# Kernel tuning notes

Measured on AMD Instinct MI355X. Metric: run time of the kernel, lower is better.

Reference implementation:

```python
import jax, jax.numpy as jnp
import numpy as np

N_ENT = 20000
N_REL = 24
N_EDGE = 200000
BATCH = 64
N_RULES = 32
RULE_LEN = 2


def setup_inputs() -> dict:
    key = jax.random.key(0)
    ks = jax.random.split(key, 9)
    return {
        "all_h": jax.random.randint(ks[0], (BATCH,), 0, N_ENT, dtype=jnp.int32),
        "all_r": jnp.zeros((BATCH,), dtype=jnp.int32),  # query relation = 0 for all queries
        "edges_to_remove": jax.random.randint(ks[1], (BATCH,), 0, N_EDGE, dtype=jnp.int32),
        "edge_heads": jax.random.randint(ks[2], (N_EDGE,), 0, N_ENT, dtype=jnp.int32),
        "edge_rels": jax.random.randint(ks[3], (N_EDGE,), 0, N_REL, dtype=jnp.int32),
        "edge_tails": jax.random.randint(ks[4], (N_EDGE,), 0, N_ENT, dtype=jnp.int32),
        "rule_bodies": jax.random.randint(ks[5], (N_RULES, RULE_LEN), 0, N_REL, dtype=jnp.int32),
        "rule_weights": jax.random.normal(ks[6], (N_RULES,), dtype=jnp.float32),
        "bias": jax.random.normal(ks[7], (N_ENT,), dtype=jnp.float32),
    }


def reference(all_h, all_r, edges_to_remove, edge_heads, edge_rels, edge_tails,
              rule_bodies, rule_weights, bias):
    n_ent = bias.shape[0]
    rule_len = rule_bodies.shape[1]
    b = all_h.shape[0]

    # edge keep-mask (edges_to_remove are dropped from the graph for this query batch)
    keep = jnp.ones((edge_heads.shape[0],), jnp.float32).at[edges_to_remove].set(0.0)

    # grounding start state: one-hot of query heads, [B, N]
    x0 = jax.nn.one_hot(all_h, n_ent, dtype=jnp.float32)

    def propagate(x, r):
        # one hop of rule grounding: route counts along edges with relation r
        w = keep * (edge_rels == r).astype(jnp.float32)      # [E]
        contrib = x[:, edge_heads] * w[None, :]              # [B, E] gather
        # scatter-add into tail entities -> [B, N]
        return jax.ops.segment_sum(contrib.T, edge_tails, num_segments=n_ent).T

    def per_rule(carry, rule):
        score, mask = carry
        body, weight = rule
        x = x0
        for l in range(rule_len):
            x = propagate(x, body[l])
        return (score + x * weight, mask + x), None

    zeros = jnp.zeros((b, n_ent), jnp.float32)
    (score, mask), _ = jax.lax.scan(per_rule, (zeros, zeros), (rule_bodies, rule_weights))

    # entity_feature == 'bias' path: score + bias, mask all True.
    # (If mask.sum()==0, score is also all-zero, so score+bias == mask+bias and
    #  (1-mask).bool() == ones: the two torch branches coincide for 'bias'.)
    out_score = score + bias[None, :]
    out_mask = jnp.ones_like(mask, dtype=bool)
    return out_score, out_mask
```

## Files before the change

### kernel.cpp

```cpp
#include <hip/hip_runtime.h>


namespace {
constexpr int kNEnt    = 20000;
constexpr int kNRel    = 24;
constexpr int kNEdge   = 200000;
constexpr int kBatch   = 64;
constexpr int kNRules  = 32;
constexpr int kWSz     = kNRel * kNRel;
constexpr int kScore4  = kBatch * kNEnt / 4;
constexpr int kOut4    = 2 * kScore4;
constexpr int kB1      = 1024;
constexpr int kT       = 256;
}

__global__ void __launch_bounds__(kT) k_init_frontier(
        const int* __restrict__ all_h,
        const int* __restrict__ rem,
        const int* __restrict__ eh,
        const int* __restrict__ er,
        const int* __restrict__ et,
        const float* __restrict__ bias,
        float* __restrict__ out,
        int* __restrict__ headptr,
        unsigned* __restrict__ nodeNext,
        unsigned long long* __restrict__ nodeBm) {
    __shared__ int sh[kBatch];
    __shared__ int srem[kBatch];
    const int t = threadIdx.x;
    if (t < kBatch) sh[t] = all_h[t];
    else if (t < 2 * kBatch) srem[t - kBatch] = rem[t - kBatch];
    __syncthreads();
    const int gid = blockIdx.x * kT + t;
    constexpr int stride = kB1 * kT;

    for (int i = gid; i < kOut4; i += stride) {
        if (i < kScore4)
            ((float4*)out)[i] = ((const float4*)bias)[i % (kNEnt / 4)];
        else
            ((float4*)out)[i] = make_float4(1.f, 1.f, 1.f, 1.f);
    }

    for (int e = gid; e < kNEdge; e += stride) {
        int h = eh[e];
        unsigned long long bm = 0ull;
        for (int b = 0; b < kBatch; b++)
            bm |= (unsigned long long)(sh[b] == h) << b;
        if (!bm) continue;
        bool removed = false;
        for (int i = 0; i < kBatch; i++) removed |= (srem[i] == e);
        if (removed) continue;
        int tail = et[e];
        int r1   = er[e];
        int old  = atomicExch(&headptr[tail], e + 1);
        unsigned nxt = (old <= 0) ? 0u : (unsigned)old;
        nodeNext[e] = nxt | ((unsigned)r1 << 24);
        nodeBm[e]   = bm;
    }
}

__global__ void __launch_bounds__(kT) k_hop2(
        const int* __restrict__ rem,
        const int* __restrict__ eh,
        const int* __restrict__ er,
        const int* __restrict__ et,
        const int* __restrict__ rb,
        const float* __restrict__ rw,
        const int* __restrict__ headptr,
        const unsigned* __restrict__ nodeNext,
        const unsigned long long* __restrict__ nodeBm,
        float* __restrict__ out) {
    __shared__ float sW[kWSz];
    __shared__ int srem[kBatch];
    const int t = threadIdx.x;
    for (int i = t; i < kWSz; i += kT) sW[i] = 0.f;
    if (t < kBatch) srem[t] = rem[t];
    __syncthreads();
    if (t < kNRules)
        atomicAdd(&sW[rb[2 * t] * kNRel + rb[2 * t + 1]], rw[t]);
    __syncthreads();

    int e = blockIdx.x * kT + t;
    if (e >= kNEdge) return;
    int h = eh[e];
    int p = headptr[h];
    if (p <= 0) return;
    bool removed = false;
    for (int i = 0; i < kBatch; i++) removed |= (srem[i] == e);
    if (removed) return;
    int r2 = er[e];
    int t2 = et[e];
    while (p > 0) {
        int e1 = p - 1;
        unsigned nx           = nodeNext[e1];
        unsigned long long bm = nodeBm[e1];
        float w = sW[((nx >> 24) & 31u) * kNRel + r2];
        while (bm) {
            int b = __ffsll(bm) - 1;
            bm &= bm - 1;
            atomicAdd(&out[b * kNEnt + t2], w);
        }
        p = (int)(nx & 0xFFFFFFu);
    }
}

extern "C" void kernel_launch(void* const* d_in, const int* in_sizes, int n_in,
                              void* d_out, int out_size, void* d_ws, size_t ws_size,
                              hipStream_t stream) {
    const int*   all_h = (const int*)d_in[0];
    const int*   rem   = (const int*)d_in[2];
    const int*   eh    = (const int*)d_in[3];
    const int*   er    = (const int*)d_in[4];
    const int*   et    = (const int*)d_in[5];
    const int*   rb    = (const int*)d_in[6];
    const float* rw    = (const float*)d_in[7];
    const float* bias  = (const float*)d_in[8];
    float* out = (float*)d_out;

    char* ws = (char*)d_ws;
    int*                headptr  = (int*)(ws + 0);
    unsigned*           nodeNext = (unsigned*)(ws + 81920);
    unsigned long long* nodeBm   = (unsigned long long*)(ws + 881920);

    hipLaunchKernelGGL(k_init_frontier, dim3(kB1), dim3(kT), 0, stream,
                       all_h, rem, eh, er, et, bias, out,
                       headptr, nodeNext, nodeBm);
    hipLaunchKernelGGL(k_hop2, dim3((kNEdge + kT - 1) / kT), dim3(kT), 0, stream,
                       rem, eh, er, et, rb, rw, headptr, nodeNext, nodeBm, out);
}
```

Baseline: 83.46 us.

## Fuse frontier build and hop-2 into one persistent kernel with grid barrier

Merges the two kernels into a single launch of 512 blocks that uses a software grid-wide barrier (atomic counter plus magic-flag reset) between building the first-hop linked lists and the second-hop scatter. This removes one kernel launch and the gap between the two kernels. In exchange it depends on all 512 blocks being co-resident. The barrier reset races, because block 0 zeroes the counter while other blocks may already be incrementing it, and on later calls the magic flag is already set, so blocks can pass before the reset. A spin limit bounds hangs but can let blocks proceed early and read incomplete lists.

```diff
diff --git a/kernel.cpp b/kernel.cpp
--- a/kernel.cpp
+++ b/kernel.cpp
@@ -8,40 +8,57 @@
 constexpr int kBatch   = 64;
 constexpr int kNRules  = 32;
 constexpr int kWSz     = kNRel * kNRel;
+constexpr int kBlocks  = 512;
+constexpr int kT       = 256;
+constexpr int kGT      = kBlocks * kT;
 constexpr int kScore4  = kBatch * kNEnt / 4;
 constexpr int kOut4    = 2 * kScore4;
-constexpr int kB1      = 1024;
-constexpr int kT       = 256;
+constexpr unsigned kMagic     = 0x5EEDF00Du;
+constexpr unsigned kSpinLimit = 1u << 22;
 }
 
-__global__ void __launch_bounds__(kT) k_init_frontier(
+__global__ void __launch_bounds__(kT, 2) k_fused(
         const int* __restrict__ all_h,
         const int* __restrict__ rem,
         const int* __restrict__ eh,
         const int* __restrict__ er,
         const int* __restrict__ et,
+        const int* __restrict__ rb,
+        const float* __restrict__ rw,
         const float* __restrict__ bias,
         float* __restrict__ out,
         int* __restrict__ headptr,
         unsigned* __restrict__ nodeNext,
-        unsigned long long* __restrict__ nodeBm) {
-    __shared__ int sh[kBatch];
-    __shared__ int srem[kBatch];
+        unsigned long long* __restrict__ nodeBm,
+        unsigned* __restrict__ barA,
+        unsigned* __restrict__ barB) {
+    __shared__ int   sh[kBatch];
+    __shared__ int   srem[kBatch];
+    __shared__ float sW[kWSz];
     const int t = threadIdx.x;
+
+    if (blockIdx.x == 0 && t == 0) {
+        __hip_atomic_store(barA, 0u, __ATOMIC_RELAXED, __HIP_MEMORY_SCOPE_AGENT);
+        __hip_atomic_store(barB, kMagic, __ATOMIC_RELEASE, __HIP_MEMORY_SCOPE_AGENT);
+    }
+
     if (t < kBatch) sh[t] = all_h[t];
     else if (t < 2 * kBatch) srem[t - kBatch] = rem[t - kBatch];
+    for (int i = t; i < kWSz; i += kT) sW[i] = 0.f;
     __syncthreads();
+    if (t < kNRules)
+        atomicAdd(&sW[rb[2 * t] * kNRel + rb[2 * t + 1]], rw[t]);
+
     const int gid = blockIdx.x * kT + t;
-    constexpr int stride = kB1 * kT;
 
-    for (int i = gid; i < kOut4; i += stride) {
+    for (int i = gid; i < kOut4; i += kGT) {
         if (i < kScore4)
             ((float4*)out)[i] = ((const float4*)bias)[i % (kNEnt / 4)];
         else
             ((float4*)out)[i] = make_float4(1.f, 1.f, 1.f, 1.f);
     }
 
-    for (int e = gid; e < kNEdge; e += stride) {
+    for (int e = gid; e < kNEdge; e += kGT) {
         int h = eh[e];
         unsigned long long bm = 0ull;
         for (int b = 0; b < kBatch; b++)
@@ -50,57 +67,52 @@
         bool removed = false;
         for (int i = 0; i < kBatch; i++) removed |= (srem[i] == e);
         if (removed) continue;
-        int tail = et[e];
-        int r1   = er[e];
-        int old  = atomicExch(&headptr[tail], e + 1);
-        unsigned nxt = (old <= 0) ? 0u : (unsigned)old;
-        nodeNext[e] = nxt | ((unsigned)r1 << 24);
+        int old = atomicExch(&headptr[et[e]], e + 1);
+        nodeNext[e] = ((old <= 0) ? 0u : (unsigned)old)
+                    | ((unsigned)er[e] << 24);
         nodeBm[e]   = bm;
     }
-}
 
-__global__ void __launch_bounds__(kT) k_hop2(
-        const int* __restrict__ rem,
-        const int* __restrict__ eh,
-        const int* __restrict__ er,
-        const int* __restrict__ et,
-        const int* __restrict__ rb,
-        const float* __restrict__ rw,
-        const int* __restrict__ headptr,
-        const unsigned* __restrict__ nodeNext,
-        const unsigned long long* __restrict__ nodeBm,
-        float* __restrict__ out) {
-    __shared__ float sW[kWSz];
-    __shared__ int srem[kBatch];
-    const int t = threadIdx.x;
-    for (int i = t; i < kWSz; i += kT) sW[i] = 0.f;
-    if (t < kBatch) srem[t] = rem[t];
+    __threadfence();
     __syncthreads();
-    if (t < kNRules)
-        atomicAdd(&sW[rb[2 * t] * kNRel + rb[2 * t + 1]], rw[t]);
+    if (t == 0) {
+        unsigned tries = 0;
+        while (__hip_atomic_load(barB, __ATOMIC_ACQUIRE,
+                                 __HIP_MEMORY_SCOPE_AGENT) != kMagic &&
+               ++tries < kSpinLimit)
+            __builtin_amdgcn_s_sleep(4);
+        __hip_atomic_fetch_add(barA, 1u, __ATOMIC_ACQ_REL,
+                               __HIP_MEMORY_SCOPE_AGENT);
+        tries = 0;
+        while (__hip_atomic_load(barA, __ATOMIC_ACQUIRE,
+                                 __HIP_MEMORY_SCOPE_AGENT) < (unsigned)kBlocks &&
+               ++tries < kSpinLimit)
+            __builtin_amdgcn_s_sleep(4);
+    }
     __syncthreads();
+    __threadfence();
 
-    int e = blockIdx.x * kT + t;
-    if (e >= kNEdge) return;
-    int h = eh[e];
-    int p = headptr[h];
-    if (p <= 0) return;
-    bool removed = false;
-    for (int i = 0; i < kBatch; i++) removed |= (srem[i] == e);
-    if (removed) return;
-    int r2 = er[e];
-    int t2 = et[e];
-    while (p > 0) {
-        int e1 = p - 1;
-        unsigned nx           = nodeNext[e1];
-        unsigned long long bm = nodeBm[e1];
-        float w = sW[((nx >> 24) & 31u) * kNRel + r2];
-        while (bm) {
-            int b = __ffsll(bm) - 1;
-            bm &= bm - 1;
-            atomicAdd(&out[b * kNEnt + t2], w);
+    for (int e = gid; e < kNEdge; e += kGT) {
+        int h = eh[e];
+        int p = headptr[h];
+        if (p <= 0) continue;
+        bool removed = false;
+        for (int i = 0; i < kBatch; i++) removed |= (srem[i] == e);
+        if (removed) continue;
+        int r2 = er[e];
+        int t2 = et[e];
+        while (p > 0) {
+            int e1 = p - 1;
+            unsigned nx           = nodeNext[e1];
+            unsigned long long bm = nodeBm[e1];
+            float w = sW[((nx >> 24) & 31u) * kNRel + r2];
+            while (bm) {
+                int b = __ffsll(bm) - 1;
+                bm &= bm - 1;
+                atomicAdd(&out[b * kNEnt + t2], w);
+            }
+            p = (int)(nx & 0xFFFFFFu);
         }
-        p = (int)(nx & 0xFFFFFFu);
     }
 }
 
@@ -119,12 +131,12 @@
 
     char* ws = (char*)d_ws;
     int*                headptr  = (int*)(ws + 0);
-    unsigned*           nodeNext = (unsigned*)(ws + 81920);
-    unsigned long long* nodeBm   = (unsigned long long*)(ws + 881920);
+    unsigned*           barA     = (unsigned*)(ws + 81920);
+    unsigned*           barB     = (unsigned*)(ws + 82048);
+    unsigned*           nodeNext = (unsigned*)(ws + 90112);
+    unsigned long long* nodeBm   = (unsigned long long*)(ws + 983040);
 
-    hipLaunchKernelGGL(k_init_frontier, dim3(kB1), dim3(kT), 0, stream,
-                       all_h, rem, eh, er, et, bias, out,
-                       headptr, nodeNext, nodeBm);
-    hipLaunchKernelGGL(k_hop2, dim3((kNEdge + kT - 1) / kT), dim3(kT), 0, stream,
-                       rem, eh, er, et, rb, rw, headptr, nodeNext, nodeBm, out);
+    hipLaunchKernelGGL(k_fused, dim3(kBlocks), dim3(kT), 0, stream,
+                       all_h, rem, eh, er, et, rb, rw, bias, out,
+                       headptr, nodeNext, nodeBm, barA, barB);
 }
```

New measurement: 180.2 us. 2.16x slower.
